# Optimization experiments

Measured on AMD Instinct MI355X. Metric: run time of the kernel, lower is better.

The kernel has to match this reference:

```python
import jax, jax.numpy as jnp
import numpy as np

GROUPS = 32
EPS = 1e-5


def setup_inputs() -> dict:
    key = jax.random.key(0)
    ks = jax.random.split(key, 8)
    B, C, H, W = 4, 512, 64, 64
    s = 1.0 / np.sqrt(C)  # conv1x1 fan-in init scale
    return {
        "x": jax.random.normal(ks[0], (B, C, H, W), dtype=jnp.float32),
        "gn_gamma": jnp.ones((C,), dtype=jnp.float32),
        "gn_beta": jnp.zeros((C,), dtype=jnp.float32),
        "wq": jax.random.normal(ks[1], (C, C), dtype=jnp.float32) * s,
        "bq": jnp.zeros((C,), dtype=jnp.float32),
        "wk": jax.random.normal(ks[2], (C, C), dtype=jnp.float32) * s,
        "bk": jnp.zeros((C,), dtype=jnp.float32),
        "wv": jax.random.normal(ks[3], (C, C), dtype=jnp.float32) * s,
        "bv": jnp.zeros((C,), dtype=jnp.float32),
    }


def reference(x, gn_gamma, gn_beta, wq, bq, wk, bk, wv, bv):
    B, C, H, W = x.shape
    N = H * W
    # GroupNorm over (channels-within-group, H, W)
    xg = x.reshape(B, GROUPS, C // GROUPS, H, W)
    mean = xg.mean(axis=(2, 3, 4), keepdims=True)
    var = xg.var(axis=(2, 3, 4), keepdims=True)
    xn = ((xg - mean) * jax.lax.rsqrt(var + EPS)).reshape(B, C, H, W)
    xn = xn * gn_gamma[None, :, None, None] + gn_beta[None, :, None, None]
    # 1x1 convs as channel matmuls over flattened spatial tokens: (B, C, N)
    xf = xn.reshape(B, C, N)
    q = jnp.einsum("oc,bcn->bon", wq, xf) + bq[None, :, None]  # (B, Co, N)
    k = jnp.einsum("oc,bcn->bon", wk, xf) + bk[None, :, None]
    v = jnp.einsum("oc,bcn->bon", wv, xf) + bv[None, :, None]
    # scores[b, m, n] = <Q_m, K_n> / sqrt(Co); full N x N matrix as in original
    scale = 1.0 / jnp.sqrt(jnp.asarray(C, dtype=x.dtype))
    scores = jnp.einsum("bcm,bcn->bmn", q, k) * scale  # (B, N, N)
    prob = jax.nn.softmax(scores, axis=-1)
    # out[b, c, m] = sum_n prob[b, m, n] * v[b, c, n]
    attn = jnp.einsum("bmn,bcn->bcm", prob, v).reshape(B, C, H, W)
    return x + attn  # ResLine is Identity since ch_in == ch_out
```

## Files before the change

### kernel.cpp

```cpp
#include <hip/hip_runtime.h>
#include <cstdint>

typedef __attribute__((ext_vector_type(8))) short short8;
typedef __attribute__((ext_vector_type(4))) float floatx4;
typedef __attribute__((ext_vector_type(8))) int intx8;

__device__ __forceinline__ unsigned short f2bf(float f) {
  unsigned int u = __float_as_uint(f);
  u += 0x7fffu + ((u >> 16) & 1u);
  return (unsigned short)(u >> 16);
}

__global__ __launch_bounds__(256) void gn_partial_kernel(
    const float* __restrict__ x, float* __restrict__ gsums) {
  const int b = blockIdx.x >> 8;
  const int g = (blockIdx.x >> 3) & 31;
  const int e = blockIdx.x & 7;
  const long long off = ((long long)(b * 512 + g * 16)) * 4096;
  const float4* xp = (const float4*)(x + off) + e * 2048;
  float s = 0.f, ss = 0.f;
  for (int i = threadIdx.x; i < 2048; i += 256) {
    float4 v = xp[i];
    s  += v.x + v.y + v.z + v.w;
    ss += v.x * v.x + v.y * v.y + v.z * v.z + v.w * v.w;
  }
  for (int off2 = 32; off2; off2 >>= 1) { s += __shfl_down(s, off2); ss += __shfl_down(ss, off2); }
  __shared__ float sb[8];
  const int lane = threadIdx.x & 63, wave = threadIdx.x >> 6;
  if (lane == 0) { sb[wave] = s; sb[4 + wave] = ss; }
  __syncthreads();
  if (threadIdx.x == 0) {
    atomicAdd(gsums + (b * 32 + g) * 2,     sb[0] + sb[1] + sb[2] + sb[3]);
    atomicAdd(gsums + (b * 32 + g) * 2 + 1, sb[4] + sb[5] + sb[6] + sb[7]);
  }
}

__global__ __launch_bounds__(256) void gn_finalize_kernel(
    const float* __restrict__ gsums, const float* __restrict__ gamma,
    const float* __restrict__ beta, float* __restrict__ scale,
    float* __restrict__ shift) {
  const int i = blockIdx.x * 256 + threadIdx.x;
  const int b = i >> 9;
  const int c = i & 511;
  const int g = c >> 4;
  const float S  = gsums[(b * 32 + g) * 2];
  const float SS = gsums[(b * 32 + g) * 2 + 1];
  const float mean = S * (1.f / 65536.f);
  const float var  = SS * (1.f / 65536.f) - mean * mean;
  const float inv  = rsqrtf(var + 1e-5f);
  const float sc = gamma[c] * inv;
  scale[i] = sc;
  shift[i] = beta[c] - mean * sc;
}

__global__ __launch_bounds__(256) void wcvt_zero_kernel(
    const float* __restrict__ wq, const float* __restrict__ wk,
    const float* __restrict__ wv, unsigned short* __restrict__ w16,
    float* __restrict__ zp, int nzero) {
  const int gi = blockIdx.x * 256 + threadIdx.x;
  if (gi < 196608) {
    const int m = gi >> 16;
    const int i = gi & 65535;
    const float* src = (m == 0) ? wq : (m == 1) ? wk : wv;
    float4 v = *((const float4*)src + i);
    ushort4 o;
    o.x = f2bf(v.x); o.y = f2bf(v.y); o.z = f2bf(v.z); o.w = f2bf(v.w);
    *((ushort4*)(w16 + (long long)m * 262144) + i) = o;
  } else {
    const int zi = gi - 196608;
    if (zi < nzero) zp[zi] = 0.f;
  }
}

__global__ __launch_bounds__(256) void norm_transpose_kernel(
    const float* __restrict__ x, const float* __restrict__ scale,
    const float* __restrict__ shift, unsigned short* __restrict__ xnt) {
  const int b = blockIdx.z;
  const int n0 = blockIdx.x * 64;
  const int c0 = blockIdx.y * 64;
  const int t = threadIdx.x;
  __shared__ unsigned short tile[64][65];
  {
    const int cl = t >> 2;
    const int nc = (t & 3) * 16;
    const int c = c0 + cl;
    const float* xp = x + ((long long)b * 512 + c) * 4096 + n0 + nc;
    const float sc = scale[b * 512 + c];
    const float sh = shift[b * 512 + c];
#pragma unroll
    for (int j = 0; j < 16; j += 4) {
      float4 v = *(const float4*)(xp + j);
      tile[cl][nc + j + 0] = f2bf(v.x * sc + sh);
      tile[cl][nc + j + 1] = f2bf(v.y * sc + sh);
      tile[cl][nc + j + 2] = f2bf(v.z * sc + sh);
      tile[cl][nc + j + 3] = f2bf(v.w * sc + sh);
    }
  }
  __syncthreads();
  {
    const int nl = t >> 2;
    const int cc = (t & 3) * 16;
    union { unsigned short u[16]; uint4 q[2]; } o;
#pragma unroll
    for (int j = 0; j < 16; ++j) o.u[j] = tile[cc + j][nl];
    unsigned short* op = xnt + ((long long)b * 4096 + n0 + nl) * 512 + c0 + cc;
    *((uint4*)op) = o.q[0];
    *((uint4*)op + 1) = o.q[1];
  }
}

template <int EPI>
__global__ __launch_bounds__(256) void gemm_tn_kernel(
    const unsigned short* __restrict__ A, const unsigned short* __restrict__ B,
    void* __restrict__ C, const float* __restrict__ bias,
    const float* __restrict__ bias2,
    int lda, int ldb, int ldc, int K,
    long long sA, long long sB, long long sC) {
  const int tid = threadIdx.x;
  const int lane = tid & 63;
  const int wave = tid >> 6;
  const int m0 = blockIdx.x * 128;
  const int n0 = blockIdx.y * 128;
  const int bz = blockIdx.z;
  A += (long long)bz * sA;
  B += (long long)bz * sB;

  __shared__ unsigned short smem[17408];
  unsigned short* As = smem;
  unsigned short* Bs = smem + 8192;

  floatx4 acc[4][4];
#pragma unroll
  for (int i = 0; i < 4; ++i)
#pragma unroll
    for (int j = 0; j < 4; ++j) acc[i][j] = (floatx4){0.f, 0.f, 0.f, 0.f};

  const unsigned short* ag[4];
  const unsigned short* bg[4];
  unsigned ldsoff[4];
#pragma unroll
  for (int i = 0; i < 4; ++i) {
    const int idx = i * 256 + tid;
    const int r = idx >> 3;
    const int g = idx & 7;
    const int gs = g ^ (r & 7);
    ag[i] = A + (long long)(m0 + r) * lda + gs * 8;
    bg[i] = B + (long long)(n0 + r) * ldb + gs * 8;
    ldsoff[i] = (unsigned)(i * 256 + wave * 64) * 8;
  }

  const int l15 = lane & 15;
  const int wm = (wave >> 1) * 64;
  const int wn = (wave & 1) * 64;

  for (int k0 = 0; k0 < K; k0 += 64) {
#pragma unroll
    for (int i = 0; i < 4; ++i) {
      __builtin_amdgcn_global_load_lds(
          (const __attribute__((address_space(1))) void*)(ag[i] + k0),
          (__attribute__((address_space(3))) void*)(As + ldsoff[i]), 16, 0, 0);
      __builtin_amdgcn_global_load_lds(
          (const __attribute__((address_space(1))) void*)(bg[i] + k0),
          (__attribute__((address_space(3))) void*)(Bs + ldsoff[i]), 16, 0, 0);
    }
    __syncthreads();
#pragma unroll
    for (int kk = 0; kk < 64; kk += 32) {
      const int gq = (kk >> 3) + (lane >> 4);
      short8 af[4], bfr[4];
#pragma unroll
      for (int mt = 0; mt < 4; ++mt) {
        const int row = wm + mt * 16 + l15;
        af[mt] = *(const short8*)&As[row * 64 + ((gq ^ (row & 7)) << 3)];
      }
#pragma unroll
      for (int nt = 0; nt < 4; ++nt) {
        const int row = wn + nt * 16 + l15;
        bfr[nt] = *(const short8*)&Bs[row * 64 + ((gq ^ (row & 7)) << 3)];
      }
#pragma unroll
      for (int mt = 0; mt < 4; ++mt)
#pragma unroll
        for (int nt = 0; nt < 4; ++nt)
          acc[mt][nt] = __builtin_amdgcn_mfma_f32_16x16x32_bf16(
              af[mt], bfr[nt], acc[mt][nt], 0, 0, 0);
    }
    __syncthreads();
  }

  const int r0 = (lane >> 4) * 4;

  if (EPI == 6) {
    unsigned char* t8 = (unsigned char*)smem;
    const float* bp = (m0 >= 512) ? bias2 : bias;
    const int mb = m0 & 511;
#pragma unroll
    for (int mt = 0; mt < 4; ++mt) {
      const int ml = wm + mt * 16 + r0;
      const float b0 = bp[mb + ml], b1 = bp[mb + ml + 1];
      const float b2 = bp[mb + ml + 2], b3 = bp[mb + ml + 3];
      const int gw = ml >> 4;
      const int mby = ml & 15;
#pragma unroll
      for (int nt = 0; nt < 4; ++nt) {
        const int nl = wn + nt * 16 + l15;
        int p = __builtin_amdgcn_cvt_pk_fp8_f32(acc[mt][nt][0] + b0,
                                                acc[mt][nt][1] + b1, 0, false);
        p = __builtin_amdgcn_cvt_pk_fp8_f32(acc[mt][nt][2] + b2,
                                            acc[mt][nt][3] + b3, p, true);
        *(int*)&t8[nl * 128 + ((gw ^ (nl & 7)) << 4) + mby] = p;
      }
    }
    __syncthreads();
    unsigned char* o8 = (unsigned char*)C + (long long)bz * sC;
#pragma unroll
    for (int t = 0; t < 4; ++t) {
      const int gid = t * 256 + tid;
      const int row = gid >> 3;
      const int gc = gid & 7;
      uint4 v = *(const uint4*)&t8[row * 128 + ((gc ^ (row & 7)) << 4)];
      *(uint4*)&o8[(long long)(n0 + row) * ldc + m0 + gc * 16] = v;
    }
    return;
  }

  if (EPI == 3) {
    unsigned char* t8 = (unsigned char*)smem;
#pragma unroll
    for (int mt = 0; mt < 4; ++mt) {
      const int ml = wm + mt * 16 + r0;
      const float b0 = bias[m0 + ml],     b1 = bias[m0 + ml + 1];
      const float b2 = bias[m0 + ml + 2], b3 = bias[m0 + ml + 3];
#pragma unroll
      for (int nt = 0; nt < 4; ++nt) {
        const int nl = wn + nt * 16 + l15;
        int p0 = __builtin_amdgcn_cvt_pk_fp8_f32(acc[mt][nt][0] + b0,
                                                 acc[mt][nt][1] + b1, 0, false);
        int p1 = __builtin_amdgcn_cvt_pk_fp8_f32(acc[mt][nt][2] + b2,
                                                 acc[mt][nt][3] + b3, 0, false);
        t8[(ml + 0) * 144 + nl] = (unsigned char)(p0 & 0xff);
        t8[(ml + 1) * 144 + nl] = (unsigned char)((p0 >> 8) & 0xff);
        t8[(ml + 2) * 144 + nl] = (unsigned char)(p1 & 0xff);
        t8[(ml + 3) * 144 + nl] = (unsigned char)((p1 >> 8) & 0xff);
      }
    }
    __syncthreads();
    unsigned char* o8 = (unsigned char*)C + (long long)bz * sC;
#pragma unroll
    for (int t = 0; t < 4; ++t) {
      const int gid = t * 256 + tid;
      const int row = gid >> 3;
      const int gc = gid & 7;
      uint4 v = *(const uint4*)&t8[row * 144 + gc * 16];
      *(uint4*)&o8[(long long)(m0 + row) * ldc + n0 + gc * 16] = v;
    }
    return;
  }
}

__global__ __launch_bounds__(512, 1) void fused_attn_kernel(
    const unsigned char* __restrict__ qk8,
    const unsigned char* __restrict__ vv8,
    float* __restrict__ out, const float* __restrict__ res) {
  const int id = blockIdx.x;
  const int xcd = id & 7;
  const int slot = id >> 3;
  const int bz = xcd & 3;
  const int n0 = ((xcd >> 2) * 32 + slot) * 64;

  const unsigned char* Q = qk8 + (long long)bz * (4096LL * 1024);
  const unsigned char* K = Q + 512;
  const unsigned char* V = vv8 + (long long)bz * (512LL * 4096);

  const int tid = threadIdx.x;
  const int lane = tid & 63;
  const int wave = tid >> 6;
  const int l15 = lane & 15;
  const int quad = lane >> 4;

  __shared__ unsigned char smem[109568];
  unsigned char* Qs = smem;
  unsigned char* Ks = smem + 32768;
  unsigned char* Ps = smem + 98304;
  float* red = (float*)(smem + 107520);

  floatx4 acc[4][4];
#pragma unroll
  for (int i = 0; i < 4; ++i)
#pragma unroll
    for (int j = 0; j < 4; ++j) acc[i][j] = (floatx4){0.f, 0.f, 0.f, 0.f};
  float rs[4] = {0.f, 0.f, 0.f, 0.f};

#define FA_GLDS(gp, lp)                                              \
  __builtin_amdgcn_global_load_lds(                                  \
      (const __attribute__((address_space(1))) void*)(gp),           \
      (__attribute__((address_space(3))) void*)(lp), 16, 0, 0)

  const unsigned char* kg[8];
  unsigned ko[8];
#pragma unroll
  for (int j = 0; j < 8; ++j) {
    const int idx = j * 512 + tid;
    const int r = idx >> 5;
    const int g = idx & 31;
    const int gs = (g & 24) | ((g & 7) ^ (r & 7));
    kg[j] = K + (long long)r * 1024 + gs * 16;
    ko[j] = 32768u + (unsigned)(j * 512 + wave * 64) * 16;
  }
  {
#pragma unroll
    for (int j = 0; j < 4; ++j) {
      const int idx = j * 512 + tid;
      const int r = idx >> 5;
      const int g = idx & 31;
      const int gs = (g & 24) | ((g & 7) ^ (r & 7));
      FA_GLDS(Q + (long long)(n0 + r) * 1024 + gs * 16,
              smem + (unsigned)(j * 512 + wave * 64) * 16);
    }
#pragma unroll
    for (int j = 0; j < 8; ++j) FA_GLDS(kg[j], smem + ko[j]);
    asm volatile("s_waitcnt vmcnt(0)" ::: "memory");
    __builtin_amdgcn_s_barrier();
  }

  const unsigned char* vg[4];
#pragma unroll
  for (int cs = 0; cs < 4; ++cs)
    vg[cs] = V + (long long)(wave * 64 + cs * 16 + l15) * 4096 + quad * 32;

  const float SCL = 0.044194173824159216f;

  for (int t = 0; t < 32; ++t) {
    const int jcol = t * 128;

    uint4 vf[4][2];
#pragma unroll
    for (int cs = 0; cs < 4; ++cs) {
      vf[cs][0] = *(const uint4*)(vg[cs] + jcol);
      vf[cs][1] = *(const uint4*)(vg[cs] + jcol + 16);
    }
    __builtin_amdgcn_sched_barrier(0);

    floatx4 sacc[4];
#pragma unroll
    for (int ns = 0; ns < 4; ++ns) sacc[ns] = (floatx4){0.f, 0.f, 0.f, 0.f};
#pragma unroll
    for (int kc = 0; kc < 4; ++kc) {
      intx8 af;
      {
        const int row = wave * 16 + l15;
        const int r7 = row & 7;
        const uint4 x0 = *(const uint4*)(Ks + row * 512 + kc * 128 +
                                         (((2 * quad) ^ r7) << 4));
        const uint4 x1 = *(const uint4*)(Ks + row * 512 + kc * 128 +
                                         (((2 * quad + 1) ^ r7) << 4));
        af = (intx8){(int)x0.x, (int)x0.y, (int)x0.z, (int)x0.w,
                     (int)x1.x, (int)x1.y, (int)x1.z, (int)x1.w};
      }
#pragma unroll
      for (int ns = 0; ns < 4; ++ns) {
        const int row = ns * 16 + l15;
        const int r7 = row & 7;
        const uint4 x0 = *(const uint4*)(Qs + row * 512 + kc * 128 +
                                         (((2 * quad) ^ r7) << 4));
        const uint4 x1 = *(const uint4*)(Qs + row * 512 + kc * 128 +
                                         (((2 * quad + 1) ^ r7) << 4));
        const intx8 bq = (intx8){(int)x0.x, (int)x0.y, (int)x0.z, (int)x0.w,
                                 (int)x1.x, (int)x1.y, (int)x1.z, (int)x1.w};
        sacc[ns] = __builtin_amdgcn_mfma_scale_f32_16x16x128_f8f6f4(
            af, bq, sacc[ns], 0, 0, 0, 127, 0, 127);
      }
    }

#pragma unroll
    for (int ns = 0; ns < 4; ++ns) {
      const float e0 = __expf(sacc[ns][0] * SCL);
      const float e1 = __expf(sacc[ns][1] * SCL);
      const float e2 = __expf(sacc[ns][2] * SCL);
      const float e3 = __expf(sacc[ns][3] * SCL);
      rs[ns] += e0 + e1 + e2 + e3;
      int p = __builtin_amdgcn_cvt_pk_fp8_f32(e0, e1, 0, false);
      p = __builtin_amdgcn_cvt_pk_fp8_f32(e2, e3, p, true);
      *(int*)&Ps[(ns * 16 + l15) * 144 + wave * 16 + quad * 4] = p;
    }
    asm volatile("s_waitcnt lgkmcnt(0)" ::: "memory");
    __builtin_amdgcn_sched_barrier(0);
    __builtin_amdgcn_s_barrier();

    if (t < 31) {
      const long long koff = (long long)(t + 1) * 131072;
#pragma unroll
      for (int j = 0; j < 8; ++j) FA_GLDS(kg[j] + koff, smem + ko[j]);
    }
    __builtin_amdgcn_sched_barrier(0);

    intx8 pb[4];
#pragma unroll
    for (int ns = 0; ns < 4; ++ns) {
      const int row = ns * 16 + l15;
      const uint4 x0 = *(const uint4*)(Ps + row * 144 + quad * 32);
      const uint4 x1 = *(const uint4*)(Ps + row * 144 + quad * 32 + 16);
      pb[ns] = (intx8){(int)x0.x, (int)x0.y, (int)x0.z, (int)x0.w,
                       (int)x1.x, (int)x1.y, (int)x1.z, (int)x1.w};
    }
    __builtin_amdgcn_s_setprio(1);
#pragma unroll
    for (int cs = 0; cs < 4; ++cs) {
      const intx8 av = (intx8){(int)vf[cs][0].x, (int)vf[cs][0].y,
                               (int)vf[cs][0].z, (int)vf[cs][0].w,
                               (int)vf[cs][1].x, (int)vf[cs][1].y,
                               (int)vf[cs][1].z, (int)vf[cs][1].w};
#pragma unroll
      for (int ns = 0; ns < 4; ++ns)
        acc[cs][ns] = __builtin_amdgcn_mfma_scale_f32_16x16x128_f8f6f4(
            av, pb[ns], acc[cs][ns], 0, 0, 0, 127, 0, 127);
    }
    __builtin_amdgcn_s_setprio(0);

    asm volatile("s_waitcnt vmcnt(0)" ::: "memory");
    __builtin_amdgcn_s_barrier();
  }
#undef FA_GLDS

#pragma unroll
  for (int ns = 0; ns < 4; ++ns) {
    float r = rs[ns];
    r += __shfl_xor(r, 16);
    r += __shfl_xor(r, 32);
    if (quad == 0) red[wave * 64 + ns * 16 + l15] = r;
  }
  __syncthreads();
  float inv[4];
#pragma unroll
  for (int ns = 0; ns < 4; ++ns) {
    float s = 0.f;
#pragma unroll
    for (int w = 0; w < 8; ++w) s += red[w * 64 + ns * 16 + l15];
    inv[ns] = 1.f / s;
  }

  float* o = out + (long long)bz * (4096LL * 512);
  const float* rr = res + (long long)bz * (4096LL * 512);
#pragma unroll
  for (int cs = 0; cs < 4; ++cs) {
#pragma unroll
    for (int ns = 0; ns < 4; ++ns) {
      const int n = n0 + ns * 16 + l15;
#pragma unroll
      for (int r = 0; r < 4; ++r) {
        const int c = wave * 64 + cs * 16 + quad * 4 + r;
        const long long off = (long long)c * 4096 + n;
        o[off] = acc[cs][ns][r] * inv[ns] + rr[off];
      }
    }
  }
}

extern "C" void kernel_launch(void* const* d_in, const int* in_sizes, int n_in,
                              void* d_out, int out_size, void* d_ws, size_t ws_size,
                              hipStream_t stream) {
  const float* x     = (const float*)d_in[0];
  const float* gamma = (const float*)d_in[1];
  const float* beta  = (const float*)d_in[2];
  const float* wq    = (const float*)d_in[3];
  const float* bq    = (const float*)d_in[4];
  const float* wk    = (const float*)d_in[5];
  const float* bk    = (const float*)d_in[6];
  const float* wv    = (const float*)d_in[7];
  const float* bv    = (const float*)d_in[8];
  float* out = (float*)d_out;

  const long long sTok = 4096LL * 512;
  const long long sQK8 = 4096LL * 1024;
  const long long sV8  = 512LL * 4096;

  char* ws = (char*)d_ws;
  float* scale = (float*)ws;
  float* shift = (float*)(ws + 8192);
  unsigned short* w16 = (unsigned short*)(ws + 16384);
  unsigned short* xnt = (unsigned short*)(ws + 1589248);
  unsigned char*  qk8 = (unsigned char*)(ws + 18366464);
  unsigned char*  vv8 = (unsigned char*)(ws + 51920896);
  float* gsums = (float*)(ws + 60317696);

  wcvt_zero_kernel<<<769, 256, 0, stream>>>(wq, wk, wv, w16, gsums, 256);
  gn_partial_kernel<<<1024, 256, 0, stream>>>(x, gsums);
  gn_finalize_kernel<<<8, 256, 0, stream>>>(gsums, gamma, beta, scale, shift);
  norm_transpose_kernel<<<dim3(64, 8, 4), 256, 0, stream>>>(x, scale, shift, xnt);

  gemm_tn_kernel<6><<<dim3(8, 32, 4), 256, 0, stream>>>(
      w16, xnt, qk8, bq, bk, 512, 512, 1024, 512, 0, sTok, sQK8);
  gemm_tn_kernel<3><<<dim3(4, 32, 4), 256, 0, stream>>>(
      w16 + 524288, xnt, vv8, bv, nullptr, 512, 512, 4096, 512, 0, sTok, sV8);

  fused_attn_kernel<<<256, 512, 0, stream>>>(qk8, vv8, out, x);
}
```

Before: 287.7 us.

## Halve attention waves, keep Q in registers, double-buffer K tiles

The fused attention kernel now runs 256 threads (4 waves) per block instead of 512. Each wave covers twice as many key rows and value channels, and the Q fragments are loaded once into registers instead of being re-read from LDS every iteration. K tiles are double-buffered in LDS and prefetched two steps ahead, with partial vmcnt waits, so global loads overlap compute. The cost is much higher register pressure (acc grows to 8x4 plus qf and 16 V fragments), which could cause spills, and less latency hiding from fewer waves.

```diff
diff --git a/kernel.cpp b/kernel.cpp
--- a/kernel.cpp
+++ b/kernel.cpp
@@ -258,7 +258,7 @@
   }
 }
 
-__global__ __launch_bounds__(512, 1) void fused_attn_kernel(
+__global__ __launch_bounds__(256, 1) void fused_attn_kernel(
     const unsigned char* __restrict__ qk8,
     const unsigned char* __restrict__ vv8,
     float* __restrict__ out, const float* __restrict__ res) {
@@ -278,15 +278,13 @@
   const int l15 = lane & 15;
   const int quad = lane >> 4;
 
-  __shared__ unsigned char smem[109568];
-  unsigned char* Qs = smem;
-  unsigned char* Ks = smem + 32768;
-  unsigned char* Ps = smem + 98304;
-  float* red = (float*)(smem + 107520);
-
-  floatx4 acc[4][4];
-#pragma unroll
-  for (int i = 0; i < 4; ++i)
+  __shared__ unsigned char smem[141312];
+  unsigned char* Ps = smem + 131072;
+  float* red = (float*)(smem + 140288);
+
+  floatx4 acc[8][4];
+#pragma unroll
+  for (int i = 0; i < 8; ++i)
 #pragma unroll
     for (int j = 0; j < 4; ++j) acc[i][j] = (floatx4){0.f, 0.f, 0.f, 0.f};
   float rs[4] = {0.f, 0.f, 0.f, 0.f};
@@ -296,101 +294,117 @@
       (const __attribute__((address_space(1))) void*)(gp),           \
       (__attribute__((address_space(3))) void*)(lp), 16, 0, 0)
 
-  const unsigned char* kg[8];
-  unsigned ko[8];
-#pragma unroll
-  for (int j = 0; j < 8; ++j) {
-    const int idx = j * 512 + tid;
-    const int r = idx >> 5;
-    const int g = idx & 31;
-    const int gs = (g & 24) | ((g & 7) ^ (r & 7));
-    kg[j] = K + (long long)r * 1024 + gs * 16;
-    ko[j] = 32768u + (unsigned)(j * 512 + wave * 64) * 16;
-  }
-  {
-#pragma unroll
-    for (int j = 0; j < 4; ++j) {
-      const int idx = j * 512 + tid;
-      const int r = idx >> 5;
-      const int g = idx & 31;
-      const int gs = (g & 24) | ((g & 7) ^ (r & 7));
-      FA_GLDS(Q + (long long)(n0 + r) * 1024 + gs * 16,
-              smem + (unsigned)(j * 512 + wave * 64) * 16);
-    }
-#pragma unroll
-    for (int j = 0; j < 8; ++j) FA_GLDS(kg[j], smem + ko[j]);
-    asm volatile("s_waitcnt vmcnt(0)" ::: "memory");
-    __builtin_amdgcn_s_barrier();
-  }
-
-  const unsigned char* vg[4];
-#pragma unroll
-  for (int cs = 0; cs < 4; ++cs)
-    vg[cs] = V + (long long)(wave * 64 + cs * 16 + l15) * 4096 + quad * 32;
+  const int r8 = tid >> 5;
+  const int g5 = tid & 31;
+  const int gsw = (g5 & 24) | ((g5 & 7) ^ (r8 & 7));
+  const unsigned char* qsrc = Q + (long long)(n0 + r8) * 1024 + gsw * 16;
+  const unsigned char* ksrc = K + (long long)r8 * 1024 + gsw * 16;
+  const unsigned dstb = (unsigned)wave * 1024;
+
+#pragma unroll
+  for (int j = 0; j < 8; ++j)
+    FA_GLDS(qsrc + j * 8192, smem + j * 4096 + dstb);
+  asm volatile("s_waitcnt vmcnt(0)" ::: "memory");
+  __builtin_amdgcn_s_barrier();
+
+  intx8 qf[4][4];
+#pragma unroll
+  for (int ns = 0; ns < 4; ++ns) {
+    const int row = ns * 16 + l15;
+    const int r7 = row & 7;
+#pragma unroll
+    for (int kc = 0; kc < 4; ++kc) {
+      const uint4 x0 = *(const uint4*)(smem + row * 512 + kc * 128 +
+                                       (((2 * quad) ^ r7) << 4));
+      const uint4 x1 = *(const uint4*)(smem + row * 512 + kc * 128 +
+                                       (((2 * quad + 1) ^ r7) << 4));
+      qf[ns][kc] = (intx8){(int)x0.x, (int)x0.y, (int)x0.z, (int)x0.w,
+                           (int)x1.x, (int)x1.y, (int)x1.z, (int)x1.w};
+    }
+  }
+  asm volatile("s_waitcnt lgkmcnt(0)" ::: "memory");
+  __builtin_amdgcn_sched_barrier(0);
+  __builtin_amdgcn_s_barrier();
+
+#pragma unroll
+  for (int j = 0; j < 16; ++j)
+    FA_GLDS(ksrc + j * 8192, smem + j * 4096 + dstb);
+#pragma unroll
+  for (int j = 0; j < 16; ++j)
+    FA_GLDS(ksrc + 131072 + j * 8192, smem + 65536 + j * 4096 + dstb);
+  asm volatile("s_waitcnt vmcnt(16)" ::: "memory");
+  __builtin_amdgcn_s_barrier();
+
+  const unsigned char* vg[8];
+#pragma unroll
+  for (int cs = 0; cs < 8; ++cs)
+    vg[cs] = V + (long long)(wave * 128 + cs * 16 + l15) * 4096 + quad * 32;
 
   const float SCL = 0.044194173824159216f;
 
   for (int t = 0; t < 32; ++t) {
+    const unsigned char* Kb = smem + (t & 1) * 65536;
     const int jcol = t * 128;
 
-    uint4 vf[4][2];
-#pragma unroll
-    for (int cs = 0; cs < 4; ++cs) {
+    uint4 vf[8][2];
+#pragma unroll
+    for (int cs = 0; cs < 8; ++cs) {
       vf[cs][0] = *(const uint4*)(vg[cs] + jcol);
       vf[cs][1] = *(const uint4*)(vg[cs] + jcol + 16);
     }
     __builtin_amdgcn_sched_barrier(0);
 
-    floatx4 sacc[4];
-#pragma unroll
-    for (int ns = 0; ns < 4; ++ns) sacc[ns] = (floatx4){0.f, 0.f, 0.f, 0.f};
+    floatx4 sacc[2][4];
+#pragma unroll
+    for (int mt = 0; mt < 2; ++mt)
+#pragma unroll
+      for (int ns = 0; ns < 4; ++ns) sacc[mt][ns] = (floatx4){0.f, 0.f, 0.f, 0.f};
 #pragma unroll
     for (int kc = 0; kc < 4; ++kc) {
-      intx8 af;
-      {
-        const int row = wave * 16 + l15;
+      intx8 kf[2];
+#pragma unroll
+      for (int mt = 0; mt < 2; ++mt) {
+        const int row = wave * 32 + mt * 16 + l15;
         const int r7 = row & 7;
-        const uint4 x0 = *(const uint4*)(Ks + row * 512 + kc * 128 +
+        const uint4 x0 = *(const uint4*)(Kb + row * 512 + kc * 128 +
                                          (((2 * quad) ^ r7) << 4));
-        const uint4 x1 = *(const uint4*)(Ks + row * 512 + kc * 128 +
+        const uint4 x1 = *(const uint4*)(Kb + row * 512 + kc * 128 +
                                          (((2 * quad + 1) ^ r7) << 4));
-        af = (intx8){(int)x0.x, (int)x0.y, (int)x0.z, (int)x0.w,
-                     (int)x1.x, (int)x1.y, (int)x1.z, (int)x1.w};
-      }
+        kf[mt] = (intx8){(int)x0.x, (int)x0.y, (int)x0.z, (int)x0.w,
+                         (int)x1.x, (int)x1.y, (int)x1.z, (int)x1.w};
+      }
+#pragma unroll
+      for (int mt = 0; mt < 2; ++mt)
+#pragma unroll
+        for (int ns = 0; ns < 4; ++ns)
+          sacc[mt][ns] = __builtin_amdgcn_mfma_scale_f32_16x16x128_f8f6f4(
+              kf[mt], qf[ns][kc], sacc[mt][ns], 0, 0, 0, 127, 0, 127);
+    }
+
+#pragma unroll
+    for (int mt = 0; mt < 2; ++mt) {
 #pragma unroll
       for (int ns = 0; ns < 4; ++ns) {
-        const int row = ns * 16 + l15;
-        const int r7 = row & 7;
-        const uint4 x0 = *(const uint4*)(Qs + row * 512 + kc * 128 +
-                                         (((2 * quad) ^ r7) << 4));
-        const uint4 x1 = *(const uint4*)(Qs + row * 512 + kc * 128 +
-                                         (((2 * quad + 1) ^ r7) << 4));
-        const intx8 bq = (intx8){(int)x0.x, (int)x0.y, (int)x0.z, (int)x0.w,
-                                 (int)x1.x, (int)x1.y, (int)x1.z, (int)x1.w};
-        sacc[ns] = __builtin_amdgcn_mfma_scale_f32_16x16x128_f8f6f4(
-            af, bq, sacc[ns], 0, 0, 0, 127, 0, 127);
-      }
-    }
-
-#pragma unroll
-    for (int ns = 0; ns < 4; ++ns) {
-      const float e0 = __expf(sacc[ns][0] * SCL);
-      const float e1 = __expf(sacc[ns][1] * SCL);
-      const float e2 = __expf(sacc[ns][2] * SCL);
-      const float e3 = __expf(sacc[ns][3] * SCL);
-      rs[ns] += e0 + e1 + e2 + e3;
-      int p = __builtin_amdgcn_cvt_pk_fp8_f32(e0, e1, 0, false);
-      p = __builtin_amdgcn_cvt_pk_fp8_f32(e2, e3, p, true);
-      *(int*)&Ps[(ns * 16 + l15) * 144 + wave * 16 + quad * 4] = p;
+        const float e0 = __expf(sacc[mt][ns][0] * SCL);
+        const float e1 = __expf(sacc[mt][ns][1] * SCL);
+        const float e2 = __expf(sacc[mt][ns][2] * SCL);
+        const float e3 = __expf(sacc[mt][ns][3] * SCL);
+        rs[ns] += e0 + e1 + e2 + e3;
+        int p = __builtin_amdgcn_cvt_pk_fp8_f32(e0, e1, 0, false);
+        p = __builtin_amdgcn_cvt_pk_fp8_f32(e2, e3, p, true);
+        *(int*)&Ps[(ns * 16 + l15) * 144 + wave * 32 + mt * 16 + quad * 4] = p;
+      }
     }
     asm volatile("s_waitcnt lgkmcnt(0)" ::: "memory");
     __builtin_amdgcn_sched_barrier(0);
     __builtin_amdgcn_s_barrier();
 
-    if (t < 31) {
-      const long long koff = (long long)(t + 1) * 131072;
-#pragma unroll
-      for (int j = 0; j < 8; ++j) FA_GLDS(kg[j] + koff, smem + ko[j]);
+    if (t < 30) {
+      const unsigned char* ks2 = ksrc + (long long)(t + 2) * 131072;
+      unsigned char* db = smem + (t & 1) * 65536;
+#pragma unroll
+      for (int j = 0; j < 16; ++j)
+        FA_GLDS(ks2 + j * 8192, db + j * 4096 + dstb);
     }
     __builtin_amdgcn_sched_barrier(0);
 
@@ -403,9 +417,15 @@
       pb[ns] = (intx8){(int)x0.x, (int)x0.y, (int)x0.z, (int)x0.w,
                        (int)x1.x, (int)x1.y, (int)x1.z, (int)x1.w};
     }
+    if (t < 30) {
+      asm volatile("s_waitcnt vmcnt(16)" ::: "memory");
+    } else {
+      asm volatile("s_waitcnt vmcnt(0)" ::: "memory");
+    }
+    __builtin_amdgcn_sched_barrier(0);
     __builtin_amdgcn_s_setprio(1);
 #pragma unroll
-    for (int cs = 0; cs < 4; ++cs) {
+    for (int cs = 0; cs < 8; ++cs) {
       const intx8 av = (intx8){(int)vf[cs][0].x, (int)vf[cs][0].y,
                                (int)vf[cs][0].z, (int)vf[cs][0].w,
                                (int)vf[cs][1].x, (int)vf[cs][1].y,
@@ -416,8 +436,8 @@
             av, pb[ns], acc[cs][ns], 0, 0, 0, 127, 0, 127);
     }
     __builtin_amdgcn_s_setprio(0);
-
-    asm volatile("s_waitcnt vmcnt(0)" ::: "memory");
+    asm volatile("s_waitcnt lgkmcnt(0)" ::: "memory");
+    __builtin_amdgcn_sched_barrier(0);
     __builtin_amdgcn_s_barrier();
   }
 #undef FA_GLDS
@@ -435,20 +455,20 @@
   for (int ns = 0; ns < 4; ++ns) {
     float s = 0.f;
 #pragma unroll
-    for (int w = 0; w < 8; ++w) s += red[w * 64 + ns * 16 + l15];
+    for (int w = 0; w < 4; ++w) s += red[w * 64 + ns * 16 + l15];
     inv[ns] = 1.f / s;
   }
 
   float* o = out + (long long)bz * (4096LL * 512);
   const float* rr = res + (long long)bz * (4096LL * 512);
 #pragma unroll
-  for (int cs = 0; cs < 4; ++cs) {
+  for (int cs = 0; cs < 8; ++cs) {
 #pragma unroll
     for (int ns = 0; ns < 4; ++ns) {
       const int n = n0 + ns * 16 + l15;
 #pragma unroll
       for (int r = 0; r < 4; ++r) {
-        const int c = wave * 64 + cs * 16 + quad * 4 + r;
+        const int c = wave * 128 + cs * 16 + quad * 4 + r;
         const long long off = (long long)c * 4096 + n;
         o[off] = acc[cs][ns][r] * inv[ns] + rr[off];
       }
@@ -493,5 +513,5 @@
   gemm_tn_kernel<3><<<dim3(4, 32, 4), 256, 0, stream>>>(
       w16 + 524288, xnt, vv8, bv, nullptr, 512, 512, 4096, 512, 0, sTok, sV8);
 
-  fused_attn_kernel<<<256, 512, 0, stream>>>(qk8, vv8, out, x);
-}
+  fused_attn_kernel<<<256, 256, 0, stream>>>(qk8, vv8, out, x);
+}
```

Result: slower. 300.4 us (+4.4%).
